# Kernel optimization log

Measured on AMD Instinct MI355X. Metric: run time of the kernel, lower is better.

The kernel has to match this reference:

```python
import jax, jax.numpy as jnp
import numpy as np

B, S, U, T = 64, 256, 1024, 512  # batch, max_sequence_size, units, output_token_length
W_SCALE = 0.02


def setup_inputs() -> dict:
    key = jax.random.key(0)
    ks = jax.random.split(key, 12)
    inp = {
        "h": jax.random.normal(ks[0], (B, S, U), jnp.float32),
        "s_0": jax.random.normal(ks[1], (B, U), jnp.float32),
        "Wy1": jax.random.normal(ks[2], (U, U), jnp.float32) * W_SCALE,
        "by1": jnp.zeros((U,), jnp.float32),
        "Wy2": jax.random.normal(ks[3], (U, T), jnp.float32) * W_SCALE,
        "by2": jnp.zeros((T,), jnp.float32),
        "We1": jax.random.normal(ks[4], (2 * U, U), jnp.float32) * W_SCALE,
        "be1": jnp.zeros((U,), jnp.float32),
        "We2": jax.random.normal(ks[5], (U, 1), jnp.float32) * W_SCALE,
        "be2": jnp.zeros((1,), jnp.float32),
        "Wf": jax.random.normal(ks[6], (T + U, U), jnp.float32) * W_SCALE,
        "bf": jnp.zeros((U,), jnp.float32),
        "Wi": jax.random.normal(ks[7], (T + U, U), jnp.float32) * W_SCALE,
        "bi": jnp.zeros((U,), jnp.float32),
        "Wg": jax.random.normal(ks[8], (T + U, U), jnp.float32) * W_SCALE,
        "bg": jnp.zeros((U,), jnp.float32),
        "Wo": jax.random.normal(ks[9], (T + U, U), jnp.float32) * W_SCALE,
        "bo": jnp.zeros((U,), jnp.float32),
    }
    return inp


def reference(h, s_0, Wy1, by1, Wy2, by2, We1, be1, We2, be2,
              Wf, bf, Wi, bi, Wg, bg, Wo, bo):
    # Precompute the h-dependent half of the first e_dense matmul once:
    # e_dense layer1 input is concat([h_i, s]) @ We1 = h_i @ We1[:U] + s @ We1[U:]
    We1_h, We1_s = We1[:U], We1[U:]
    h_proj = jnp.einsum('bsu,uv->bsv', h, We1_h)  # [B,S,U]

    def step(s, _):
        # y_dense: U -> U (tanh) -> T (linear)
        y = jnp.tanh(s @ Wy1 + by1) @ Wy2 + by2  # [B,T]
        # additive attention scores over all S encoder positions (vectorized)
        e1 = jax.nn.sigmoid(h_proj + (s @ We1_s + be1)[:, None, :])  # [B,S,U]
        e = jax.nn.sigmoid(jnp.squeeze(e1 @ We2, -1) + be2)          # [B,S]
        a = jax.nn.softmax(e, axis=-1)
        c = jnp.einsum('bsu,bs->bu', h, a)  # context vector [B,U]
        # LSTM cell with x = y, h = s, c = attention context
        x_h = jnp.concatenate([y, s], axis=-1)  # [B,T+U]
        i = jax.nn.sigmoid(x_h @ Wi + bi)
        f = jax.nn.sigmoid(x_h @ Wf + bf)
        o = jax.nn.sigmoid(x_h @ Wo + bo)
        g = jnp.tanh(x_h @ Wg + bg)
        c_new = f * c + i * g
        s_next = o * jnp.tanh(c_new)
        return s_next, y

    _, ys = jax.lax.scan(step, s_0, None, length=S)  # ys: [S,B,T]
    return jnp.transpose(ys, (1, 0, 2))  # [B,S,T]
```

## Files before the change

### kernel.cpp

```cpp
#include <hip/hip_runtime.h>
#include <hip/hip_bf16.h>

typedef __attribute__((ext_vector_type(4))) float floatx4;
typedef __attribute__((ext_vector_type(2))) float floatx2;
typedef __attribute__((ext_vector_type(8))) short shortx8;

#define NB 64
#define NS 256
#define NU 1024
#define NT 512

__device__ __forceinline__ unsigned short f2bf(float f){
  union{float f;unsigned u;}v; v.f=f;
  unsigned r = v.u + 0x7fffu + ((v.u>>16)&1u);
  return (unsigned short)(r>>16);
}
__device__ __forceinline__ float bf2f(unsigned short h){
  union{unsigned u;float f;}v; v.u = ((unsigned)h)<<16; return v.f;
}
__device__ __forceinline__ float sigf(float x){
  return __builtin_amdgcn_rcpf(1.f + __expf(-x));
}

__device__ __forceinline__ floatx4 cld_f32x4(const float* p){
  floatx4 v;
  asm volatile("global_load_dwordx4 %0, %1, off sc0 sc1\n\ts_waitcnt vmcnt(0)"
               : "=&v"(v) : "v"(p) : "memory");
  return v;
}
__device__ __forceinline__ void cburst4d2(floatx2 o[4], const float* p0, const float* p1,
                                          const float* p2, const float* p3){
  asm volatile(
    "global_load_dwordx2 %0, %4, off sc0 sc1\n\t"
    "global_load_dwordx2 %1, %5, off sc0 sc1\n\t"
    "global_load_dwordx2 %2, %6, off sc0 sc1\n\t"
    "global_load_dwordx2 %3, %7, off sc0 sc1\n\t"
    "s_waitcnt vmcnt(0)"
    : "=&v"(o[0]),"=&v"(o[1]),"=&v"(o[2]),"=&v"(o[3])
    : "v"(p0),"v"(p1),"v"(p2),"v"(p3) : "memory");
}
__device__ __forceinline__ float cld_f32(const float* p){
  float v;
  asm volatile("global_load_dword %0, %1, off sc0 sc1\n\ts_waitcnt vmcnt(0)"
               : "=&v"(v) : "v"(p) : "memory");
  return v;
}
__device__ __forceinline__ void cst_u16(unsigned short* p, unsigned short v){
  asm volatile("global_store_short %0, %1, off sc0 sc1" :: "v"(p), "v"((unsigned)v) : "memory");
}
__device__ __forceinline__ void cst_f32(float* p, float v){
  asm volatile("global_store_dword %0, %1, off sc0 sc1" :: "v"(p), "v"(v) : "memory");
}
__device__ __forceinline__ void cst_u32(unsigned* p, unsigned v){
  asm volatile("global_store_dword %0, %1, off sc0 sc1" :: "v"(p), "v"(v) : "memory");
}

template<int MODE>
__global__ void gemm_sw(const unsigned short* __restrict__ A,
                        const unsigned short* __restrict__ Bsw,
                        void* __restrict__ Cout,
                        int M, int N, int K, int ldc,
                        const float* __restrict__ bias)
{
  const int lane = threadIdx.x & 63;
  const int lm = lane & 15, quad = lane >> 4;
  const int nwaves = (gridDim.x * blockDim.x) >> 6;
  const int w = (blockIdx.x * blockDim.x + threadIdx.x) >> 6;
  const int m64 = M >> 6, n64 = N >> 6, KS = K >> 5;
  const int ntask = m64 * n64;
  for (int task = w; task < ntask; task += nwaves) {
    const int mt = task % m64, nt = task / m64;
    floatx4 acc[4][4];
#pragma unroll
    for (int i=0;i<4;i++)
#pragma unroll
      for(int j=0;j<4;j++) acc[i][j] = (floatx4){0.f,0.f,0.f,0.f};
    const unsigned short* Ab = A + (size_t)(mt*64 + lm) * K + quad*8;
    for (int ks=0; ks<KS; ++ks) {
      shortx8 a[4], b[4];
#pragma unroll
      for (int i=0;i<4;i++)
        a[i] = *(const shortx8*)(Ab + (size_t)i*16*K + ks*32);
#pragma unroll
      for (int j=0;j<4;j++)
        b[j] = *(const shortx8*)(Bsw + (((size_t)(nt*4+j)*KS + ks)*64 + lane)*8);
#pragma unroll
      for (int i=0;i<4;i++)
#pragma unroll
        for (int j=0;j<4;j++)
          acc[i][j] = __builtin_amdgcn_mfma_f32_16x16x32_bf16(a[i], b[j], acc[i][j], 0,0,0);
    }
#pragma unroll
    for (int i=0;i<4;i++){
#pragma unroll
      for (int j=0;j<4;j++){
        const int col = nt*64 + j*16 + lm;
        const float bv = bias ? bias[col] : 0.f;
#pragma unroll
        for (int r=0;r<4;r++){
          const int row = mt*64 + i*16 + quad*4 + r;
          const float v = acc[i][j][r] + bv;
          if (MODE==0)      ((float*)Cout)[(size_t)row*ldc + col] = v;
          else if (MODE==1) ((unsigned short*)Cout)[(size_t)row*ldc + col] = f2bf(v);
          else { const int orow = (row&63)*NS + (row>>6);
                 ((float*)Cout)[(size_t)orow*ldc + col] = v; }
        }
      }
    }
  }
}

__global__ void conv_h(const float* __restrict__ src, unsigned short* __restrict__ dst, int n){
  for (int i = blockIdx.x*blockDim.x + threadIdx.x; i < n; i += gridDim.x*blockDim.x)
    dst[i] = f2bf(src[i]);
}

__global__ void conv_misc(const float* __restrict__ Wy2, const float* __restrict__ We2,
                          const float* __restrict__ s0, const float* __restrict__ by1,
                          const float* __restrict__ be1,
                          unsigned short* __restrict__ Wy2A, unsigned short* __restrict__ we2b,
                          unsigned short* __restrict__ s_bf, float* __restrict__ bz)
{
  int i = blockIdx.x*blockDim.x + threadIdx.x;
  if (i < 524288) Wy2A[i] = f2bf(Wy2[i]);
  else if (i < 525312) we2b[i-524288] = f2bf(We2[i-524288]);
  else if (i < 590848) s_bf[i-525312] = f2bf(s0[i-525312]);
  else if (i < 592896) { int n = i - 590848; bz[n] = (n<1024)? by1[n] : be1[n-1024]; }
}

__global__ void vbias_k(const float* __restrict__ by2,
                        const float* __restrict__ bi, const float* __restrict__ bff,
                        const float* __restrict__ bg, const float* __restrict__ bo,
                        const float* __restrict__ Wi, const float* __restrict__ Wf,
                        const float* __restrict__ Wg, const float* __restrict__ Wo,
                        float* __restrict__ vb)
{
  int i = blockIdx.x*blockDim.x + threadIdx.x;
  if (i >= 4096) return;
  int g = i >> 10, u = i & 1023;
  const float* bsrc = (g==0)?bi:(g==1)?bff:(g==2)?bg:bo;
  const float* W    = (g==0)?Wi:(g==1)?Wf:(g==2)?Wg:Wo;
  float s = bsrc[u];
  for (int tt = 0; tt < NT; ++tt) s += by2[tt] * W[(size_t)tt*NU + u];
  vb[i] = s;
}

__global__ void pack_b(const float* __restrict__ src, unsigned short* __restrict__ dst, int K, int N)
{
  const int KS = K >> 5;
  const size_t total = (size_t)K * N;
  for (size_t i = (size_t)blockIdx.x*blockDim.x + threadIdx.x; i < total;
       i += (size_t)gridDim.x*blockDim.x) {
    int j = i & 7; int lane = (i>>3) & 63; int r = (int)(i >> 9);
    int ks = r % KS; int nt = r / KS;
    int k = ks*32 + (lane>>4)*8 + j;
    int n = nt*16 + (lane&15);
    dst[i] = f2bf(src[(size_t)k*N + n]);
  }
}

__global__ void pack_a1(const float* __restrict__ Wy1, const float* __restrict__ We1,
                        unsigned short* __restrict__ dst)
{
  const int KS = 32;
  const size_t total = (size_t)1024*2048;
  for (size_t i = (size_t)blockIdx.x*blockDim.x + threadIdx.x; i < total;
       i += (size_t)gridDim.x*blockDim.x) {
    int j = i & 7; int lane = (i>>3) & 63; int r = (int)(i >> 9);
    int ks = r % KS; int nt = r / KS;
    int k = ks*32 + (lane>>4)*8 + j;
    int n = nt*16 + (lane&15);
    float v = (n < 1024) ? Wy1[(size_t)k*1024 + n]
                         : We1[(size_t)(1024+k)*1024 + (n-1024)];
    dst[i] = f2bf(v);
  }
}

__global__ void pack_wbig(const float* __restrict__ Mg,
                          const float* __restrict__ Wi, const float* __restrict__ Wf,
                          const float* __restrict__ Wg, const float* __restrict__ Wo,
                          unsigned short* __restrict__ dst)
{
  const int KS = 64;
  const size_t total = (size_t)2048*4096;
  for (size_t i = (size_t)blockIdx.x*blockDim.x + threadIdx.x; i < total;
       i += (size_t)gridDim.x*blockDim.x) {
    int j = i & 7; int lane = (i>>3) & 63; int r = (int)(i >> 9);
    int ks = r % KS; int nt = r / KS;
    int k = ks*32 + (lane>>4)*8 + j;
    int n = nt*16 + (lane&15);
    int g = n >> 10, u = n & 1023;
    float v;
    if (k < 1024) v = Mg[(size_t)g*1048576 + (size_t)k*1024 + u];
    else {
      const float* W = (g==0)?Wi:(g==1)?Wf:(g==2)?Wg:Wo;
      v = W[(size_t)(512 + k - 1024)*1024 + u];
    }
    dst[i] = f2bf(v);
  }
}

struct LoopArgs {
  unsigned short* s_all;
  unsigned short* tanh_all;
  const unsigned short* A1_sw;
  const unsigned short* Wbig_sw;
  const unsigned short* hproj;
  const float* h;
  const unsigned short* we2b;
  float* qbuf;
  float* watt;
  float* gates;
  const float* bz;
  const float* vbias;
  const float* be2;
  int* bar;
};

__global__ void __launch_bounds__(1024) loop_kernel(LoopArgs A)
{
  const int tid = threadIdx.x;
  const int bid = blockIdx.x;
  const int wid = tid >> 6;
  const int lane = tid & 63;
  const int lm = lane & 15, quad = lane >> 4;

  extern __shared__ floatx4 dynlds_v4[];
  unsigned char* const dynlds = (unsigned char*)dynlds_v4;

  int* gcnt = A.bar;
  int* root = A.bar + 16*32;
  int* genp = A.bar + 16*32 + 32;

  __shared__ float qsh[1024];
  __shared__ floatx4 pbuf[256];
  __shared__ float wsh[256];
  __shared__ float zparts[4];
  __shared__ floatx2 cbuf[1024];

  auto gsync = [&]() {
    asm volatile("s_waitcnt vmcnt(0) lgkmcnt(0)" ::: "memory");
    __syncthreads();
    if (tid == 0) {
      int g = __hip_atomic_load(genp, __ATOMIC_RELAXED, __HIP_MEMORY_SCOPE_AGENT);
      int grp = bid >> 4;
      if (__hip_atomic_fetch_add(&gcnt[grp*32], 1, __ATOMIC_RELAXED, __HIP_MEMORY_SCOPE_AGENT) == 15) {
        __hip_atomic_store(&gcnt[grp*32], 0, __ATOMIC_RELAXED, __HIP_MEMORY_SCOPE_AGENT);
        if (__hip_atomic_fetch_add(root, 1, __ATOMIC_RELAXED, __HIP_MEMORY_SCOPE_AGENT) == 15) {
          __hip_atomic_store(root, 0, __ATOMIC_RELAXED, __HIP_MEMORY_SCOPE_AGENT);
          __hip_atomic_store(genp, g + 1, __ATOMIC_RELAXED, __HIP_MEMORY_SCOPE_AGENT);
        }
      }
      while (__hip_atomic_load(genp, __ATOMIC_RELAXED, __HIP_MEMORY_SCOPE_AGENT) == g)
        __builtin_amdgcn_s_sleep(1);
    }
    __syncthreads();
  };

  const int b3 = bid >> 2;
  const int j0_blk = (bid & 3) << 6;
  const int u3 = ((bid & 3) << 8) + (tid & 127) * 2;
  const int js3 = (tid >> 7) << 5;

  unsigned hreg[32];
  {
    const float* hb = A.h + (size_t)b3*NS*NU;
#pragma unroll
    for (int jj = 0; jj < 32; ++jj) {
      const floatx2 hv = *(const floatx2*)(hb + (size_t)(js3 + jj)*NU + u3);
      hreg[jj] = ((unsigned)f2bf(hv[0])) | (((unsigned)f2bf(hv[1])) << 16);
    }
  }
  {
    const unsigned char* hpg = (const unsigned char*)(A.hproj + ((size_t)(b3*NS + j0_blk))*NU);
#pragma unroll
    for (int it = 0; it < 8; ++it)
      *(floatx4*)(dynlds + it*16384 + tid*16) = *(const floatx4*)(hpg + it*16384 + tid*16);
  }
  float w2r[16];
  if (wid >= 8) {
    const shortx8 wa = *(const shortx8*)(A.we2b + 8*lane);
    const shortx8 wb = *(const shortx8*)(A.we2b + 512 + 8*lane);
#pragma unroll
    for (int i = 0; i < 8; ++i) {
      w2r[i]   = bf2f((unsigned short)wa[i]);
      w2r[8+i] = bf2f((unsigned short)wb[i]);
    }
  }
  const float be2v = A.be2[0];
  __syncthreads();

#pragma clang loop unroll(disable)
  for (int t = 0; t < NS; ++t) {
    const unsigned short* sbase = A.s_all + (size_t)t*(NB*NU);
    {
      floatx4 accg = (floatx4){0.f,0.f,0.f,0.f};
      if (wid < 4) {
        const int task = bid*2 + (wid & 1);
        const int mt = task & 3, nt = task >> 2;
        const int kh = wid >> 1;
        floatx4 acc = (floatx4){0.f,0.f,0.f,0.f};
        const unsigned short* Ab = sbase + (mt*16 + lm)*NU + quad*8;
        for (int k = 0; k < 2; ++k) {
          const int kb = kh*2 + k;
          shortx8 a[8];
#pragma unroll
          for (int q = 0; q < 8; ++q) a[q] = *(const shortx8*)(Ab + kb*256 + q*32);
#pragma unroll
          for (int q = 0; q < 8; ++q) {
            shortx8 b = *(const shortx8*)(A.A1_sw + (((size_t)nt*32 + kb*8 + q)*64 + lane)*8);
            acc = __builtin_amdgcn_mfma_f32_16x16x32_bf16(a[q], b, acc, 0,0,0);
          }
        }
        if (wid >= 2) pbuf[(wid-2)*64 + lane] = acc; else accg = acc;
      }
      __syncthreads();
      if (wid < 2) {
        const int task = bid*2 + wid;
        const int mt = task & 3, nt = task >> 2;
        floatx4 acc = accg + pbuf[wid*64 + lane];
        const int col = nt*16 + lm;
        const float bzv = A.bz[col];
#pragma unroll
        for (int r = 0; r < 4; ++r) {
          const int row = mt*16 + quad*4 + r;
          const float v = acc[r] + bzv;
          if (col < NU) cst_u16(A.tanh_all + (size_t)t*(NB*NU) + row*NU + col, f2bf(tanhf(v)));
          else          cst_f32(A.qbuf + row*NU + (col - NU), v);
        }
      }
    }
    gsync();
    {
      if (tid >= 512 && tid < 768) {
        const int i = tid - 512;
        *(floatx4*)&qsh[i*4] = cld_f32x4(A.qbuf + b3*NU + i*4);
      }
      __syncthreads();
      floatx4 accg = (floatx4){0.f,0.f,0.f,0.f};
      if (wid < 8) {
        const int mt = wid & 3, nt = bid;
        const int sel = wid >> 2;
        floatx4 acc = (floatx4){0.f,0.f,0.f,0.f};
        const int arow = mt*16 + lm;
        const unsigned short* aA =
            (sel ? sbase : A.tanh_all + (size_t)t*(NB*NU)) + arow*NU + quad*8;
        const int bofs = sel ? 32 : 0;
        for (int kb = 0; kb < 4; ++kb) {
          shortx8 a[8];
#pragma unroll
          for (int q = 0; q < 8; ++q) a[q] = *(const shortx8*)(aA + kb*256 + q*32);
#pragma unroll
          for (int q = 0; q < 8; ++q) {
            shortx8 b = *(const shortx8*)(A.Wbig_sw + (((size_t)nt*64 + bofs + kb*8 + q)*64 + lane)*8);
            acc = __builtin_amdgcn_mfma_f32_16x16x32_bf16(a[q], b, acc, 0,0,0);
          }
        }
        if (sel) pbuf[(wid-4)*64 + lane] = acc; else accg = acc;
      } else {
        const int rbase = (wid - 8) * 8;
        float qv[16];
#pragma unroll
        for (int i = 0; i < 8; ++i) {
          qv[i]   = qsh[8*lane + i];
          qv[8+i] = qsh[512 + 8*lane + i];
        }
        for (int jj = 0; jj < 8; ++jj) {
          const int rl = rbase + jj;
          const shortx8 h0 = *(const shortx8*)(dynlds + rl*2048 + lane*16);
          const shortx8 h1 = *(const shortx8*)(dynlds + rl*2048 + 1024 + lane*16);
          float dot = 0.f;
#pragma unroll
          for (int i = 0; i < 8; ++i) {
            const float x = bf2f((unsigned short)h0[i]) + qv[i];
            dot += w2r[i] * sigf(x);
          }
#pragma unroll
          for (int i = 0; i < 8; ++i) {
            const float x = bf2f((unsigned short)h1[i]) + qv[8+i];
            dot += w2r[8+i] * sigf(x);
          }
#pragma unroll
          for (int off = 32; off > 0; off >>= 1) dot += __shfl_down(dot, off, 64);
          if (lane == 0) {
            const float e = 1.f/(1.f + __expf(-(dot + be2v)));
            cst_f32(A.watt + b3*NS + (j0_blk + rl), __expf(e));
          }
        }
      }
      __syncthreads();
      if (wid < 4) {
        floatx4 acc = accg + pbuf[wid*64 + lane];
        const int col = bid*16 + lm;
        const float vb = A.vbias[col];
#pragma unroll
        for (int r = 0; r < 4; ++r) {
          const int row = (wid&3)*16 + quad*4 + r;
          cst_f32(A.gates + row*4096 + col, acc[r] + vb);
        }
      }
    }
    gsync();
    {
      const int b = b3, uc = (bid & 3) << 8;
      if (tid < 256) wsh[tid] = cld_f32(A.watt + b*NS + tid);
      __syncthreads();
      if (wid < 4) {
        float z = wsh[wid*64 + lane];
#pragma unroll
        for (int off = 32; off > 0; off >>= 1) z += __shfl_down(z, off, 64);
        if (lane == 0) zparts[wid] = z;
      }
      __syncthreads();
      const float invZ = __builtin_amdgcn_rcpf(zparts[0]+zparts[1]+zparts[2]+zparts[3]);
      float c0 = 0.f, c1 = 0.f;
#pragma unroll
      for (int jj = 0; jj < 32; ++jj) {
        const unsigned hv = hreg[jj];
        const float wv = wsh[js3 + jj];
        c0 += wv * bf2f((unsigned short)(hv & 0xffffu));
        c1 += wv * bf2f((unsigned short)(hv >> 16));
      }
      cbuf[tid] = (floatx2){c0, c1};
      __syncthreads();
      if (tid < 128) {
        float cc0 = 0.f, cc1 = 0.f;
#pragma unroll
        for (int k = 0; k < 8; ++k) {
          const floatx2 v = cbuf[tid + (k << 7)];
          cc0 += v[0]; cc1 += v[1];
        }
        cc0 *= invZ; cc1 *= invZ;
        const int uu = uc + tid*2;
        const float* gp = A.gates + b*4096;
        floatx2 g4[4];
        cburst4d2(g4, gp + uu, gp + NU + uu, gp + 2*NU + uu, gp + 3*NU + uu);
        unsigned sout = 0;
#pragma unroll
        for (int p = 0; p < 2; ++p) {
          const float cx = p ? cc1 : cc0;
          const float iv = sigf(g4[0][p]);
          const float fv = sigf(g4[1][p]);
          const float gv = tanhf(g4[2][p]);
          const float ov = sigf(g4[3][p]);
          const float cn = fv*cx + iv*gv;
          const float sn = ov * tanhf(cn);
          sout |= ((unsigned)f2bf(sn)) << (16*p);
        }
        cst_u32((unsigned*)(A.s_all + (size_t)(t+1)*(NB*NU) + b*NU + uu), sout);
      }
    }
    gsync();
  }
}

extern "C" void kernel_launch(void* const* d_in, const int* in_sizes, int n_in,
                              void* d_out, int out_size, void* d_ws, size_t ws_size,
                              hipStream_t stream)
{
  const float* h   = (const float*)d_in[0];
  const float* s0  = (const float*)d_in[1];
  const float* Wy1 = (const float*)d_in[2];
  const float* by1 = (const float*)d_in[3];
  const float* Wy2 = (const float*)d_in[4];
  const float* by2 = (const float*)d_in[5];
  const float* We1 = (const float*)d_in[6];
  const float* be1 = (const float*)d_in[7];
  const float* We2 = (const float*)d_in[8];
  const float* be2 = (const float*)d_in[9];
  const float* Wf_p = (const float*)d_in[10];
  const float* bf_p = (const float*)d_in[11];
  const float* Wi_p = (const float*)d_in[12];
  const float* bi_p = (const float*)d_in[13];
  const float* Wg_p = (const float*)d_in[14];
  const float* bg_p = (const float*)d_in[15];
  const float* Wo_p = (const float*)d_in[16];
  const float* bo_p = (const float*)d_in[17];
  (void)in_sizes; (void)n_in; (void)out_size; (void)ws_size;

  char* ws = (char*)d_ws;
  size_t off = 0;
  auto alloc = [&](size_t bytes)->char*{
    char* p = ws + off; off = (off + bytes + 255) & ~(size_t)255; return p;
  };
  unsigned short* h_bf    = (unsigned short*)alloc((size_t)NB*NS*NU*2);
  unsigned short* hproj   = (unsigned short*)alloc((size_t)NB*NS*NU*2);
  unsigned short* tanh_all= (unsigned short*)alloc((size_t)NS*NB*NU*2);
  unsigned short* s_all   = (unsigned short*)alloc((size_t)(NS+1)*NB*NU*2);
  unsigned short* A1_sw   = (unsigned short*)alloc((size_t)NU*2048*2);
  unsigned short* Wbig_sw = (unsigned short*)alloc((size_t)2048*4096*2);
  unsigned short* We1h_sw = (unsigned short*)alloc((size_t)NU*NU*2);
  unsigned short* Wy2_sw  = (unsigned short*)alloc((size_t)NU*NT*2);
  unsigned short* we2b = (unsigned short*)alloc(NU*2);
  float* qbuf  = (float*)alloc((size_t)NB*NU*4);
  float* watt  = (float*)alloc((size_t)NB*NS*4);
  float* gates = (float*)alloc((size_t)NB*4096*4);
  float* bz    = (float*)alloc(2048*4);
  float* vbias = (float*)alloc(4096*4);
  int*   bar   = (int*)alloc(4096);
  float* Mg = (float*)tanh_all;
  unsigned short* Wy2A    = hproj;
  unsigned short* Wgtop_sw= hproj + (size_t)NU*NT;

  hipMemsetAsync(bar, 0, 4096, stream);

  conv_h<<<dim3(4096), dim3(256), 0, stream>>>(h, h_bf, NB*NS*NU);
  conv_misc<<<dim3(2316), dim3(256), 0, stream>>>(Wy2, We2, s0, by1, be1, Wy2A, we2b, s_all, bz);
  vbias_k<<<dim3(16), dim3(256), 0, stream>>>(by2, bi_p, bf_p, bg_p, bo_p,
                                              Wi_p, Wf_p, Wg_p, Wo_p, vbias);
  pack_b<<<dim3(1024), dim3(256), 0, stream>>>(We1, We1h_sw, 1024, 1024);
  pack_b<<<dim3(1024), dim3(256), 0, stream>>>(Wy2, Wy2_sw, 1024, 512);
  pack_b<<<dim3(512), dim3(256), 0, stream>>>(Wi_p, Wgtop_sw + 0*((size_t)NT*NU), 512, 1024);
  pack_b<<<dim3(512), dim3(256), 0, stream>>>(Wf_p, Wgtop_sw + 1*((size_t)NT*NU), 512, 1024);
  pack_b<<<dim3(512), dim3(256), 0, stream>>>(Wg_p, Wgtop_sw + 2*((size_t)NT*NU), 512, 1024);
  pack_b<<<dim3(512), dim3(256), 0, stream>>>(Wo_p, Wgtop_sw + 3*((size_t)NT*NU), 512, 1024);
  pack_a1<<<dim3(1024), dim3(256), 0, stream>>>(Wy1, We1, A1_sw);

  for (int g = 0; g < 4; ++g)
    gemm_sw<0><<<dim3(1024), dim3(256), 0, stream>>>(
        Wy2A, Wgtop_sw + (size_t)g*(NT*NU), Mg + (size_t)g*NU*NU,
        1024, 1024, 512, 1024, nullptr);
  pack_wbig<<<dim3(2048), dim3(256), 0, stream>>>(Mg, Wi_p, Wf_p, Wg_p, Wo_p, Wbig_sw);

  gemm_sw<1><<<dim3(1024), dim3(256), 0, stream>>>(
      h_bf, We1h_sw, hproj, NB*NS, 1024, 1024, 1024, nullptr);

  LoopArgs la;
  la.s_all = s_all; la.tanh_all = tanh_all; la.A1_sw = A1_sw; la.Wbig_sw = Wbig_sw;
  la.hproj = hproj; la.h = h; la.we2b = we2b;
  la.qbuf = qbuf; la.watt = watt; la.gates = gates;
  la.bz = bz; la.vbias = vbias; la.be2 = be2; la.bar = bar;
  loop_kernel<<<dim3(256), dim3(1024), 131072, stream>>>(la);

  gemm_sw<2><<<dim3(1024), dim3(256), 0, stream>>>(
      tanh_all, Wy2_sw, d_out, NB*NS, 512, 1024, 512, by2);
}
```

Measured before the change: 12.27 ms.

## Cache per-block Wbig slice in LDS, split hproj between LDS and registers, remap XCD tasks

Each block loads its Wbig weight slice into LDS once before the time loop, so the per-step gate matmul reads B operands from LDS instead of global memory. To make room, the hproj tile is split: the first half of each row stays in LDS and the second half is held in registers per attention wave. The first-phase task mapping is changed so blocks on the same XCD share a column tile of A1, which should improve L2 locality. The cost is higher register pressure and more LDS use.

```diff
diff --git a/kernel.cpp b/kernel.cpp
--- a/kernel.cpp
+++ b/kernel.cpp
@@ -227,6 +227,7 @@
 
   extern __shared__ floatx4 dynlds_v4[];
   unsigned char* const dynlds = (unsigned char*)dynlds_v4;
+  unsigned char* const ldsW   = dynlds + 65536;
 
   int* gcnt = A.bar;
   int* root = A.bar + 16*32;
@@ -274,11 +275,25 @@
   {
     const unsigned char* hpg = (const unsigned char*)(A.hproj + ((size_t)(b3*NS + j0_blk))*NU);
 #pragma unroll
-    for (int it = 0; it < 8; ++it)
-      *(floatx4*)(dynlds + it*16384 + tid*16) = *(const floatx4*)(hpg + it*16384 + tid*16);
-  }
+    for (int it = 0; it < 4; ++it) {
+      const int o = it*16384 + tid*16;
+      const int rl = o >> 10, ub = o & 1023;
+      *(floatx4*)(dynlds + o) = *(const floatx4*)(hpg + (size_t)rl*2048 + ub);
+    }
+    const unsigned char* wbs = (const unsigned char*)A.Wbig_sw + (size_t)bid*65536;
+#pragma unroll
+    for (int it = 0; it < 4; ++it) {
+      const int o = it*16384 + tid*16;
+      *(floatx4*)(ldsW + o) = *(const floatx4*)(wbs + o);
+    }
+  }
+  shortx8 hp2[8];
   float w2r[16];
   if (wid >= 8) {
+    const int rbase = (wid - 8) * 8;
+    const unsigned short* hpg2 = A.hproj + (size_t)(b3*NS + j0_blk + rbase)*NU + 512 + 8*lane;
+#pragma unroll
+    for (int r = 0; r < 8; ++r) hp2[r] = *(const shortx8*)(hpg2 + (size_t)r*NU);
     const shortx8 wa = *(const shortx8*)(A.we2b + 8*lane);
     const shortx8 wb = *(const shortx8*)(A.we2b + 512 + 8*lane);
 #pragma unroll
@@ -294,10 +309,11 @@
   for (int t = 0; t < NS; ++t) {
     const unsigned short* sbase = A.s_all + (size_t)t*(NB*NU);
     {
+      const int xcd = bid & 7, kk = bid >> 3;
+      const int ntp1 = (kk >> 1)*8 + xcd;
       floatx4 accg = (floatx4){0.f,0.f,0.f,0.f};
       if (wid < 4) {
-        const int task = bid*2 + (wid & 1);
-        const int mt = task & 3, nt = task >> 2;
+        const int mt = (kk & 1)*2 + (wid & 1);
         const int kh = wid >> 1;
         floatx4 acc = (floatx4){0.f,0.f,0.f,0.f};
         const unsigned short* Ab = sbase + (mt*16 + lm)*NU + quad*8;
@@ -308,7 +324,7 @@
           for (int q = 0; q < 8; ++q) a[q] = *(const shortx8*)(Ab + kb*256 + q*32);
 #pragma unroll
           for (int q = 0; q < 8; ++q) {
-            shortx8 b = *(const shortx8*)(A.A1_sw + (((size_t)nt*32 + kb*8 + q)*64 + lane)*8);
+            shortx8 b = *(const shortx8*)(A.A1_sw + (((size_t)ntp1*32 + kb*8 + q)*64 + lane)*8);
             acc = __builtin_amdgcn_mfma_f32_16x16x32_bf16(a[q], b, acc, 0,0,0);
           }
         }
@@ -316,10 +332,9 @@
       }
       __syncthreads();
       if (wid < 2) {
-        const int task = bid*2 + wid;
-        const int mt = task & 3, nt = task >> 2;
+        const int mt = (kk & 1)*2 + wid;
         floatx4 acc = accg + pbuf[wid*64 + lane];
-        const int col = nt*16 + lm;
+        const int col = ntp1*16 + lm;
         const float bzv = A.bz[col];
 #pragma unroll
         for (int r = 0; r < 4; ++r) {
@@ -339,7 +354,7 @@
       __syncthreads();
       floatx4 accg = (floatx4){0.f,0.f,0.f,0.f};
       if (wid < 8) {
-        const int mt = wid & 3, nt = bid;
+        const int mt = wid & 3;
         const int sel = wid >> 2;
         floatx4 acc = (floatx4){0.f,0.f,0.f,0.f};
         const int arow = mt*16 + lm;
@@ -352,7 +367,7 @@
           for (int q = 0; q < 8; ++q) a[q] = *(const shortx8*)(aA + kb*256 + q*32);
 #pragma unroll
           for (int q = 0; q < 8; ++q) {
-            shortx8 b = *(const shortx8*)(A.Wbig_sw + (((size_t)nt*64 + bofs + kb*8 + q)*64 + lane)*8);
+            shortx8 b = *(const shortx8*)(ldsW + ((bofs + kb*8 + q)*64 + lane)*16);
             acc = __builtin_amdgcn_mfma_f32_16x16x32_bf16(a[q], b, acc, 0,0,0);
           }
         }
@@ -365,10 +380,10 @@
           qv[i]   = qsh[8*lane + i];
           qv[8+i] = qsh[512 + 8*lane + i];
         }
+#pragma unroll
         for (int jj = 0; jj < 8; ++jj) {
           const int rl = rbase + jj;
-          const shortx8 h0 = *(const shortx8*)(dynlds + rl*2048 + lane*16);
-          const shortx8 h1 = *(const shortx8*)(dynlds + rl*2048 + 1024 + lane*16);
+          const shortx8 h0 = *(const shortx8*)(dynlds + rl*1024 + lane*16);
           float dot = 0.f;
 #pragma unroll
           for (int i = 0; i < 8; ++i) {
@@ -377,7 +392,7 @@
           }
 #pragma unroll
           for (int i = 0; i < 8; ++i) {
-            const float x = bf2f((unsigned short)h1[i]) + qv[8+i];
+            const float x = bf2f((unsigned short)hp2[jj][i]) + qv[8+i];
             dot += w2r[8+i] * sigf(x);
           }
 #pragma unroll
```

New measurement: 13.97 ms. +13.9%, slower.

## Hoist s-dependent gate matmul into phase one and remap tasks by XCD

Applied to the files above, without the earlier changes.

The s-half of the LSTM gate matmul depends only on the current state, so it moves into the first phase of each step. Idle waves 4-7 compute it there alongside the y/attention projection, which shortens the critical path of the second phase. The first-phase task mapping is also changed so blocks sharing an XCD handle the same weight column tile, aiming for better L2 reuse of weights. It costs more registers to carry acc_s across the grid sync.

```diff
diff --git a/kernel.cpp b/kernel.cpp
--- a/kernel.cpp
+++ b/kernel.cpp
@@ -293,11 +293,13 @@
 #pragma clang loop unroll(disable)
   for (int t = 0; t < NS; ++t) {
     const unsigned short* sbase = A.s_all + (size_t)t*(NB*NU);
+    floatx4 acc_s = (floatx4){0.f,0.f,0.f,0.f};
     {
+      const int xcd = bid & 7, kk = bid >> 3;
+      const int ntp1 = (kk >> 1)*8 + xcd;
       floatx4 accg = (floatx4){0.f,0.f,0.f,0.f};
       if (wid < 4) {
-        const int task = bid*2 + (wid & 1);
-        const int mt = task & 3, nt = task >> 2;
+        const int mt = (kk & 1)*2 + (wid & 1);
         const int kh = wid >> 1;
         floatx4 acc = (floatx4){0.f,0.f,0.f,0.f};
         const unsigned short* Ab = sbase + (mt*16 + lm)*NU + quad*8;
@@ -308,18 +310,30 @@
           for (int q = 0; q < 8; ++q) a[q] = *(const shortx8*)(Ab + kb*256 + q*32);
 #pragma unroll
           for (int q = 0; q < 8; ++q) {
-            shortx8 b = *(const shortx8*)(A.A1_sw + (((size_t)nt*32 + kb*8 + q)*64 + lane)*8);
+            shortx8 b = *(const shortx8*)(A.A1_sw + (((size_t)ntp1*32 + kb*8 + q)*64 + lane)*8);
             acc = __builtin_amdgcn_mfma_f32_16x16x32_bf16(a[q], b, acc, 0,0,0);
           }
         }
         if (wid >= 2) pbuf[(wid-2)*64 + lane] = acc; else accg = acc;
+      } else if (wid < 8) {
+        const int mt = wid - 4;
+        const unsigned short* sA = sbase + (mt*16 + lm)*NU + quad*8;
+        for (int kb = 0; kb < 4; ++kb) {
+          shortx8 a[8];
+#pragma unroll
+          for (int q = 0; q < 8; ++q) a[q] = *(const shortx8*)(sA + kb*256 + q*32);
+#pragma unroll
+          for (int q = 0; q < 8; ++q) {
+            shortx8 b = *(const shortx8*)(A.Wbig_sw + (((size_t)bid*64 + 32 + kb*8 + q)*64 + lane)*8);
+            acc_s = __builtin_amdgcn_mfma_f32_16x16x32_bf16(a[q], b, acc_s, 0,0,0);
+          }
+        }
       }
       __syncthreads();
       if (wid < 2) {
-        const int task = bid*2 + wid;
-        const int mt = task & 3, nt = task >> 2;
+        const int mt = (kk & 1)*2 + wid;
         floatx4 acc = accg + pbuf[wid*64 + lane];
-        const int col = nt*16 + lm;
+        const int col = ntp1*16 + lm;
         const float bzv = A.bz[col];
 #pragma unroll
         for (int r = 0; r < 4; ++r) {
@@ -337,27 +351,22 @@
         *(floatx4*)&qsh[i*4] = cld_f32x4(A.qbuf + b3*NU + i*4);
       }
       __syncthreads();
-      floatx4 accg = (floatx4){0.f,0.f,0.f,0.f};
-      if (wid < 8) {
-        const int mt = wid & 3, nt = bid;
-        const int sel = wid >> 2;
+      if (wid < 4) {
+        const int mt = wid;
         floatx4 acc = (floatx4){0.f,0.f,0.f,0.f};
-        const int arow = mt*16 + lm;
-        const unsigned short* aA =
-            (sel ? sbase : A.tanh_all + (size_t)t*(NB*NU)) + arow*NU + quad*8;
-        const int bofs = sel ? 32 : 0;
+        const unsigned short* tA = A.tanh_all + (size_t)t*(NB*NU) + (mt*16 + lm)*NU + quad*8;
         for (int kb = 0; kb < 4; ++kb) {
           shortx8 a[8];
 #pragma unroll
-          for (int q = 0; q < 8; ++q) a[q] = *(const shortx8*)(aA + kb*256 + q*32);
+          for (int q = 0; q < 8; ++q) a[q] = *(const shortx8*)(tA + kb*256 + q*32);
 #pragma unroll
           for (int q = 0; q < 8; ++q) {
-            shortx8 b = *(const shortx8*)(A.Wbig_sw + (((size_t)nt*64 + bofs + kb*8 + q)*64 + lane)*8);
+            shortx8 b = *(const shortx8*)(A.Wbig_sw + (((size_t)bid*64 + kb*8 + q)*64 + lane)*8);
             acc = __builtin_amdgcn_mfma_f32_16x16x32_bf16(a[q], b, acc, 0,0,0);
           }
         }
-        if (sel) pbuf[(wid-4)*64 + lane] = acc; else accg = acc;
-      } else {
+        pbuf[wid*64 + lane] = acc;
+      } else if (wid >= 8) {
         const int rbase = (wid - 8) * 8;
         float qv[16];
 #pragma unroll
@@ -389,13 +398,13 @@
         }
       }
       __syncthreads();
-      if (wid < 4) {
-        floatx4 acc = accg + pbuf[wid*64 + lane];
+      if (wid >= 4 && wid < 8) {
+        floatx4 acc = acc_s + pbuf[(wid-4)*64 + lane];
         const int col = bid*16 + lm;
         const float vb = A.vbias[col];
 #pragma unroll
         for (int r = 0; r < 4; ++r) {
-          const int row = (wid&3)*16 + quad*4 + r;
+          const int row = (wid-4)*16 + quad*4 + r;
           cst_f32(A.gates + row*4096 + col, acc[r] + vb);
         }
       }
```

After: 14.70 ms. 19.8% more time.
